# Kernel tuning notes

Measured on AMD Instinct MI355X. Metric: run time of the kernel, lower is better.

Reference implementation:

```python
import jax, jax.numpy as jnp
import numpy as np


def _squash(t, axis):
    # matches torch: t / norm * (norm^2 / (1 + norm^2))
    ns = jnp.sum(t * t, axis=axis, keepdims=True)
    norm = jnp.sqrt(ns)
    return t / norm * (ns / (1.0 + ns))


def setup_inputs() -> dict:
    key = jax.random.key(0)
    k1, k2 = jax.random.split(key)
    B, I, A_IN, O, A_OUT = 16, 2048, 16, 64, 32
    x = jax.random.normal(k1, (B, I, A_IN, 1), dtype=jnp.float32)
    # nn.init.normal(std=0.1)
    weights = jax.random.normal(k2, (I, A_IN, O * A_OUT), dtype=jnp.float32) * 0.1
    # nn.init.constant(val=0.1)
    bias = jnp.full((O, A_OUT), 0.1, dtype=jnp.float32)
    return {"x": x, "weights": weights, "bias": bias}


def reference(x, weights, bias):
    B = x.shape[0]
    I, A_IN, OA = weights.shape
    O, A = bias.shape
    NUM_ROUTING = 3  # hardcoded in the torch forward

    # votes = sum over input_atoms of broadcast(x) * weights  -> [B, I, O, A]
    votes = jnp.einsum('bia,iaj->bij', x[..., 0], weights).reshape(B, I, O, A)
    votes_sg = jax.lax.stop_gradient(votes)

    logits = jnp.zeros((B, I, O), dtype=votes.dtype)
    activation = None
    for i in range(NUM_ROUTING):
        route = jax.nn.softmax(logits, axis=2)  # over output_dim
        v = votes if i == NUM_ROUTING - 1 else votes_sg
        # weighted sum over input capsules: [B, O, A]
        preactivate = jnp.einsum('bio,bioa->boa', route, v) + bias
        activation = _squash(preactivate, axis=2)
        if i < NUM_ROUTING - 1:
            # agreement between votes and current output capsules
            distances = jnp.einsum('bioa,boa->bio', votes, activation)
            logits = logits + distances
    return activation
```

## Files before the change

### kernel.cpp

```cpp
#include <hip/hip_runtime.h>
#include <math.h>

#define B_   16
#define I_   2048
#define AIN_ 16
#define O_   64
#define J_   2048
#define JP_  1024

__device__ __forceinline__ unsigned bf16rne(float f) {
  unsigned u = __float_as_uint(f);
  return (u + 0x7FFFu + ((u >> 16) & 1u)) >> 16;
}
__device__ __forceinline__ float bf16lo(unsigned p) { return __uint_as_float(p << 16); }
__device__ __forceinline__ float bf16hi(unsigned p) { return __uint_as_float(p & 0xFFFF0000u); }

__device__ __forceinline__ float2 ntload2(const float2* p) {
  union { double d; float2 f; } u;
  u.d = __builtin_nontemporal_load((const double*)p);
  return u.f;
}

__global__ __launch_bounds__(512) void votes_kernel(
    const float* __restrict__ x, const float* __restrict__ W,
    unsigned* __restrict__ votes)
{
  __shared__ float x_lds[8 * B_ * AIN_];
  const int tid = threadIdx.x;
  const int islab = blockIdx.x >> 1, jt = blockIdx.x & 1;
  const int i0 = islab * 8;

  for (int e = tid; e < 8 * B_ * AIN_; e += 512) {
    int b = e >> 7, il = (e >> 4) & 7, a = e & 15;
    x_lds[il * 256 + b * 16 + a] =
        x[(size_t)b * (I_ * AIN_) + (size_t)(i0 + il) * AIN_ + a];
  }
  __syncthreads();

  const float2* __restrict__ Wq = (const float2*)W;
  const int jp = jt * 512 + tid;

  for (int il = 0; il < 8; ++il) {
    const int i = i0 + il;
    const float2* __restrict__ Wi = Wq + (size_t)i * (AIN_ * JP_) + jp;
    const float2* __restrict__ xq = (const float2*)x_lds + il * 128;

    float2 v[16];
    #pragma unroll
    for (int b = 0; b < 16; ++b) v[b] = make_float2(0.f, 0.f);

    #pragma unroll
    for (int a2 = 0; a2 < 8; ++a2) {
      float2 w0 = ntload2(Wi + (size_t)(2 * a2 + 0) * JP_);
      float2 w1 = ntload2(Wi + (size_t)(2 * a2 + 1) * JP_);
      #pragma unroll
      for (int b = 0; b < 16; ++b) {
        float2 xv = xq[b * 8 + a2];
        v[b].x = fmaf(xv.x, w0.x, v[b].x);
        v[b].y = fmaf(xv.x, w0.y, v[b].y);
        v[b].x = fmaf(xv.y, w1.x, v[b].x);
        v[b].y = fmaf(xv.y, w1.y, v[b].y);
      }
    }

    unsigned* __restrict__ vo = votes + (size_t)i * (B_ * JP_) + jp;
    #pragma unroll
    for (int b = 0; b < 16; ++b)
      vo[(size_t)b * JP_] = bf16rne(v[b].x) | (bf16rne(v[b].y) << 16);
  }
}

__global__ __launch_bounds__(256) void reduce0_kernel(
    const unsigned* __restrict__ votes, const float* __restrict__ bias,
    float* __restrict__ act)
{
  __shared__ float2 red[4][64];
  const int b = blockIdx.x >> 4, jt = blockIdx.x & 15;
  const int jl = threadIdx.x & 63, is = threadIdx.x >> 6;
  const int jp = jt * 64 + jl;
  const unsigned* __restrict__ vp = votes + (size_t)b * JP_ + jp;

  float2 s0 = make_float2(0.f, 0.f), s1 = make_float2(0.f, 0.f);
  #pragma unroll 4
  for (int k = 0; k < 512; k += 2) {
    unsigned u0 = vp[(size_t)(is + 4 * k)     * (B_ * JP_)];
    unsigned u1 = vp[(size_t)(is + 4 * k + 4) * (B_ * JP_)];
    s0.x += bf16lo(u0); s0.y += bf16hi(u0);
    s1.x += bf16lo(u1); s1.y += bf16hi(u1);
  }
  red[is][jl] = make_float2(s0.x + s1.x, s0.y + s1.y);
  __syncthreads();

  if (threadIdx.x < 64) {
    float2 r0 = red[0][jl], r1 = red[1][jl], r2 = red[2][jl], r3 = red[3][jl];
    const float2 bq = ((const float2*)bias)[jp];
    float px = (r0.x + r1.x + r2.x + r3.x) * (1.0f / 64.0f) + bq.x;
    float py = (r0.y + r1.y + r2.y + r3.y) * (1.0f / 64.0f) + bq.y;
    float ns = px * px + py * py;
    ns += __shfl_xor(ns, 1);  ns += __shfl_xor(ns, 2);
    ns += __shfl_xor(ns, 4);  ns += __shfl_xor(ns, 8);
    float sc = sqrtf(ns) / (1.0f + ns);
    ((float2*)act)[(size_t)b * JP_ + jp] = make_float2(px * sc, py * sc);
  }
}

template<int PASS>
__global__ __launch_bounds__(512) void route_kernel(
    const uint2* __restrict__ votes2, const float* __restrict__ act_in,
    float* __restrict__ part, float* __restrict__ logits)
{
  __shared__ float d_lds[4 * O_];
  __shared__ float r_lds[4 * O_];

  const int jq = threadIdx.x;
  const int islab = blockIdx.x >> 2, bq = blockIdx.x & 3;
  const int i0 = islab * 8;
  const int o = jq >> 3;
  const int l8 = jq & 7;
  const float4* __restrict__ actq = (const float4*)act_in;

  float4 av[4];
  #pragma unroll
  for (int bb = 0; bb < 4; ++bb)
    av[bb] = actq[(size_t)(bq * 4 + bb) * 512 + jq];

  float4 acc[4];
  #pragma unroll
  for (int bb = 0; bb < 4; ++bb) acc[bb] = make_float4(0.f, 0.f, 0.f, 0.f);

  for (int il = 0; il < 8; ++il) {
    const int i = i0 + il;
    const uint2* __restrict__ vo =
        votes2 + (size_t)i * (B_ * 512) + (size_t)(bq * 4) * 512 + jq;
    uint2 vp[4];
    #pragma unroll
    for (int bb = 0; bb < 4; ++bb) vp[bb] = vo[(size_t)bb * 512];

    #pragma unroll
    for (int bb = 0; bb < 4; ++bb) {
      float c = bf16lo(vp[bb].x) * av[bb].x + bf16hi(vp[bb].x) * av[bb].y
              + bf16lo(vp[bb].y) * av[bb].z + bf16hi(vp[bb].y) * av[bb].w;
      c += __shfl_xor(c, 1);  c += __shfl_xor(c, 2);  c += __shfl_xor(c, 4);
      if (l8 == bb) d_lds[bb * 64 + o] = c;
    }
    __syncthreads();

    if (threadIdx.x < 256) {
      const int bb2 = threadIdx.x >> 6, o2 = threadIdx.x & 63;
      const int b2  = bq * 4 + bb2;
      float ell = d_lds[threadIdx.x];
      if (PASS == 2) ell += logits[((size_t)b2 * I_ + i) * O_ + o2];
      if (PASS == 1) logits[((size_t)b2 * I_ + i) * O_ + o2] = ell;
      float m = ell;
      m = fmaxf(m, __shfl_xor(m, 32)); m = fmaxf(m, __shfl_xor(m, 16));
      m = fmaxf(m, __shfl_xor(m, 8));  m = fmaxf(m, __shfl_xor(m, 4));
      m = fmaxf(m, __shfl_xor(m, 2));  m = fmaxf(m, __shfl_xor(m, 1));
      float e = __expf(ell - m);
      float s = e;
      s += __shfl_xor(s, 32); s += __shfl_xor(s, 16); s += __shfl_xor(s, 8);
      s += __shfl_xor(s, 4);  s += __shfl_xor(s, 2);  s += __shfl_xor(s, 1);
      r_lds[threadIdx.x] = e / s;
    }
    __syncthreads();

    #pragma unroll
    for (int bb = 0; bb < 4; ++bb) {
      float r = r_lds[bb * 64 + o];
      acc[bb].x = fmaf(r, bf16lo(vp[bb].x), acc[bb].x);
      acc[bb].y = fmaf(r, bf16hi(vp[bb].x), acc[bb].y);
      acc[bb].z = fmaf(r, bf16lo(vp[bb].y), acc[bb].z);
      acc[bb].w = fmaf(r, bf16hi(vp[bb].y), acc[bb].w);
    }
  }

  float4* __restrict__ po =
      (float4*)part + (size_t)blockIdx.x * (4 * 512) + jq;
  #pragma unroll
  for (int bb = 0; bb < 4; ++bb)
    po[(size_t)bb * 512] = acc[bb];
}

__global__ __launch_bounds__(256) void reduce_squash(
    const float* __restrict__ part, const float* __restrict__ bias,
    float* __restrict__ out)
{
  const int wave = (blockIdx.x * 256 + threadIdx.x) >> 6;
  const int L = threadIdx.x & 63;
  const int a = L & 31, q = L >> 5;
  const int b = wave >> 6, o = wave & 63;
  const int j = o * 32 + a;
  const float* __restrict__ base = part + (size_t)b * J_ + j;

  float s0 = 0.f, s1 = 0.f;
  #pragma unroll 4
  for (int k = 0; k < 128; k += 2) {
    s0 += base[(size_t)(q * 128 + k)     * (B_ * J_)];
    s1 += base[(size_t)(q * 128 + k + 1) * (B_ * J_)];
  }
  float s = s0 + s1;
  s += __shfl_xor(s, 32);

  float p = s + bias[j];
  float ns = p * p;
  ns += __shfl_xor(ns, 1);  ns += __shfl_xor(ns, 2);
  ns += __shfl_xor(ns, 4);  ns += __shfl_xor(ns, 8);
  ns += __shfl_xor(ns, 16);
  if (L < 32) out[(size_t)b * J_ + j] = p * sqrtf(ns) / (1.0f + ns);
}

template<int PASS>
__global__ __launch_bounds__(1024) void fb_pass_kernel(
    const float* __restrict__ x, const float* __restrict__ W,
    const float* __restrict__ act_in, float* __restrict__ part,
    float* __restrict__ logits)
{
  __shared__ float x_lds[8 * B_ * AIN_];
  __shared__ float d_lds[8 * O_];
  __shared__ float r_lds[8 * O_];
  const int tid = threadIdx.x, blk = blockIdx.x, i0 = blk * 8;
  for (int e = tid; e < 8 * B_ * AIN_; e += 1024) {
    int b = e >> 7, il = (e >> 4) & 7, a = e & 15;
    x_lds[il * 256 + b * 16 + a] =
        x[(size_t)b * (I_ * AIN_) + (size_t)(i0 + il) * AIN_ + a];
  }
  __syncthreads();
  const int og = tid >> 4, lg = tid & 15;
  float2 acc[16];
  #pragma unroll
  for (int b = 0; b < 16; ++b) acc[b] = make_float2(0.f, 0.f);
  const float2* __restrict__ Wq   = (const float2*)W;
  const float2* __restrict__ actq = (const float2*)act_in;
  for (int il = 0; il < 8; ++il) {
    const int i = i0 + il;
    const float2* __restrict__ Wi = Wq + (size_t)i * (AIN_ * JP_);
    const float4* __restrict__ xq = (const float4*)x_lds + il * 64;
    for (int h = 0; h < 2; ++h) {
      float2 v[8];
      #pragma unroll
      for (int bb = 0; bb < 8; ++bb) v[bb] = make_float2(0.f, 0.f);
      #pragma unroll
      for (int a4 = 0; a4 < 4; ++a4) {
        float2 w0 = Wi[(size_t)(a4 * 4 + 0) * JP_ + tid];
        float2 w1 = Wi[(size_t)(a4 * 4 + 1) * JP_ + tid];
        float2 w2 = Wi[(size_t)(a4 * 4 + 2) * JP_ + tid];
        float2 w3 = Wi[(size_t)(a4 * 4 + 3) * JP_ + tid];
        #pragma unroll
        for (int bb = 0; bb < 8; ++bb) {
          float4 xv = xq[(h * 8 + bb) * 4 + a4];
          v[bb].x = fmaf(xv.x, w0.x, v[bb].x); v[bb].y = fmaf(xv.x, w0.y, v[bb].y);
          v[bb].x = fmaf(xv.y, w1.x, v[bb].x); v[bb].y = fmaf(xv.y, w1.y, v[bb].y);
          v[bb].x = fmaf(xv.z, w2.x, v[bb].x); v[bb].y = fmaf(xv.z, w2.y, v[bb].y);
          v[bb].x = fmaf(xv.w, w3.x, v[bb].x); v[bb].y = fmaf(xv.w, w3.y, v[bb].y);
        }
      }
      if (PASS == 0) {
        #pragma unroll
        for (int bb = 0; bb < 8; ++bb) {
          acc[h * 8 + bb].x += v[bb].x; acc[h * 8 + bb].y += v[bb].y;
        }
      } else {
        #pragma unroll
        for (int bb = 0; bb < 8; ++bb) {
          const int b = h * 8 + bb;
          float2 avv = actq[(size_t)b * JP_ + tid];
          float c = v[bb].x * avv.x + v[bb].y * avv.y;
          c += __shfl_xor(c, 1); c += __shfl_xor(c, 2);
          c += __shfl_xor(c, 4); c += __shfl_xor(c, 8);
          if (lg == bb) d_lds[bb * 64 + og] = c;
        }
        __syncthreads();
        if (tid < 512) {
          const int bb2 = tid >> 6, o2 = tid & 63;
          const int b2  = h * 8 + bb2;
          float ell = d_lds[tid];
          if (PASS == 2) ell += logits[((size_t)b2 * I_ + i) * O_ + o2];
          if (PASS == 1) logits[((size_t)b2 * I_ + i) * O_ + o2] = ell;
          float m = ell;
          m = fmaxf(m, __shfl_xor(m, 32)); m = fmaxf(m, __shfl_xor(m, 16));
          m = fmaxf(m, __shfl_xor(m, 8));  m = fmaxf(m, __shfl_xor(m, 4));
          m = fmaxf(m, __shfl_xor(m, 2));  m = fmaxf(m, __shfl_xor(m, 1));
          float e = __expf(ell - m);
          float s = e;
          s += __shfl_xor(s, 32); s += __shfl_xor(s, 16); s += __shfl_xor(s, 8);
          s += __shfl_xor(s, 4);  s += __shfl_xor(s, 2);  s += __shfl_xor(s, 1);
          r_lds[tid] = e / s;
        }
        __syncthreads();
        #pragma unroll
        for (int bb = 0; bb < 8; ++bb) {
          float r = r_lds[bb * 64 + og];
          acc[h * 8 + bb].x = fmaf(r, v[bb].x, acc[h * 8 + bb].x);
          acc[h * 8 + bb].y = fmaf(r, v[bb].y, acc[h * 8 + bb].y);
        }
      }
    }
  }
  const float sc = (PASS == 0) ? (1.0f / 64.0f) : 1.0f;
  #pragma unroll
  for (int b = 0; b < 16; ++b) {
    float2* __restrict__ po = (float2*)part +
        (size_t)blk * (B_ * JP_) + (size_t)b * JP_ + tid;
    *po = make_float2(acc[b].x * sc, acc[b].y * sc);
  }
}

extern "C" void kernel_launch(void* const* d_in, const int* in_sizes, int n_in,
                              void* d_out, int out_size, void* d_ws, size_t ws_size,
                              hipStream_t stream) {
  const float* x    = (const float*)d_in[0];
  const float* W    = (const float*)d_in[1];
  const float* bias = (const float*)d_in[2];
  float* out = (float*)d_out;

  float*    part   = (float*)d_ws;
  float*    act    = part + (size_t)256 * (B_ * J_);
  float*    logits = act + (B_ * J_);
  unsigned* votes  = (unsigned*)(logits + (size_t)B_ * I_ * O_);
  const size_t need = ((size_t)256 * B_ * J_ + B_ * J_ + (size_t)B_ * I_ * O_) * 4
                    + (size_t)I_ * B_ * JP_ * 4;

  if (ws_size >= need) {
    votes_kernel<<<512, 512, 0, stream>>>(x, W, votes);
    reduce0_kernel<<<256, 256, 0, stream>>>(votes, bias, act);
    route_kernel<1><<<1024, 512, 0, stream>>>((const uint2*)votes, act, part, logits);
    reduce_squash<<<256, 256, 0, stream>>>(part, bias, act);
    route_kernel<2><<<1024, 512, 0, stream>>>((const uint2*)votes, act, part, logits);
    reduce_squash<<<256, 256, 0, stream>>>(part, bias, out);
  } else {
    fb_pass_kernel<0><<<256, 1024, 0, stream>>>(x, W, act, part, logits);
    reduce_squash<<<256, 256, 0, stream>>>(part, bias, act);
    fb_pass_kernel<1><<<256, 1024, 0, stream>>>(x, W, act, part, logits);
    reduce_squash<<<256, 256, 0, stream>>>(part, bias, act);
    fb_pass_kernel<2><<<256, 1024, 0, stream>>>(x, W, act, part, logits);
    reduce_squash<<<256, 256, 0, stream>>>(part, bias, out);
  }
}
```

Baseline: 199.0 us.

## Widen grids and vectorize vote loads across votes, route and reduce kernels

The votes kernel now handles 4 input capsules per block instead of 8, so it launches twice as many blocks. The reduce0, route and reduce_squash kernels are reorganised to read votes and partials as 16-byte uint4/float4 vectors. Route blocks shrink to 256 threads covering 2 batches each, and the reductions split work over more blocks with an LDS tree at the end. The aim is more parallelism and wider memory transactions on the bandwidth-bound passes. The cost is more partial-sum blocks and different LDS reduction patterns.

```diff
diff --git a/kernel.cpp b/kernel.cpp
--- a/kernel.cpp
+++ b/kernel.cpp
@@ -25,13 +25,14 @@
     const float* __restrict__ x, const float* __restrict__ W,
     unsigned* __restrict__ votes)
 {
-  __shared__ float x_lds[8 * B_ * AIN_];
+  __shared__ float x_lds[4 * B_ * AIN_];
   const int tid = threadIdx.x;
   const int islab = blockIdx.x >> 1, jt = blockIdx.x & 1;
-  const int i0 = islab * 8;
-
-  for (int e = tid; e < 8 * B_ * AIN_; e += 512) {
-    int b = e >> 7, il = (e >> 4) & 7, a = e & 15;
+  const int i0 = islab * 4;
+
+  for (int e = tid; e < 4 * B_ * AIN_; e += 512) {
+    int b = e >> 5 & 15, il = e >> 9, a = e & 15;
+    il = e >> 8; b = (e >> 4) & 15; a = e & 15;
     x_lds[il * 256 + b * 16 + a] =
         x[(size_t)b * (I_ * AIN_) + (size_t)(i0 + il) * AIN_ + a];
   }
@@ -40,7 +41,7 @@
   const float2* __restrict__ Wq = (const float2*)W;
   const int jp = jt * 512 + tid;
 
-  for (int il = 0; il < 8; ++il) {
+  for (int il = 0; il < 4; ++il) {
     const int i = i0 + il;
     const float2* __restrict__ Wi = Wq + (size_t)i * (AIN_ * JP_) + jp;
     const float2* __restrict__ xq = (const float2*)x_lds + il * 128;
@@ -71,141 +72,157 @@
 }
 
 __global__ __launch_bounds__(256) void reduce0_kernel(
-    const unsigned* __restrict__ votes, const float* __restrict__ bias,
+    const uint4* __restrict__ votes4, const float* __restrict__ bias,
     float* __restrict__ act)
 {
-  __shared__ float2 red[4][64];
-  const int b = blockIdx.x >> 4, jt = blockIdx.x & 15;
-  const int jl = threadIdx.x & 63, is = threadIdx.x >> 6;
-  const int jp = jt * 64 + jl;
-  const unsigned* __restrict__ vp = votes + (size_t)b * JP_ + jp;
-
-  float2 s0 = make_float2(0.f, 0.f), s1 = make_float2(0.f, 0.f);
-  #pragma unroll 4
-  for (int k = 0; k < 512; k += 2) {
-    unsigned u0 = vp[(size_t)(is + 4 * k)     * (B_ * JP_)];
-    unsigned u1 = vp[(size_t)(is + 4 * k + 4) * (B_ * JP_)];
-    s0.x += bf16lo(u0); s0.y += bf16hi(u0);
-    s1.x += bf16lo(u1); s1.y += bf16hi(u1);
-  }
-  red[is][jl] = make_float2(s0.x + s1.x, s0.y + s1.y);
+  __shared__ float red[64][4][8];
+  const int b = blockIdx.x >> 6, o = blockIdx.x & 63;
+  const int t = threadIdx.x, s = t >> 2, q = t & 3;
+  const uint4* __restrict__ vp = votes4 + (size_t)b * 256 + (size_t)(o * 4 + q);
+
+  float a0=0.f,a1=0.f,a2=0.f,a3=0.f,a4=0.f,a5=0.f,a6=0.f,a7=0.f;
+  #pragma unroll 8
+  for (int k = 0; k < 32; ++k) {
+    uint4 u = vp[(size_t)(s + 64 * k) * 4096];
+    a0 += bf16lo(u.x); a1 += bf16hi(u.x);
+    a2 += bf16lo(u.y); a3 += bf16hi(u.y);
+    a4 += bf16lo(u.z); a5 += bf16hi(u.z);
+    a6 += bf16lo(u.w); a7 += bf16hi(u.w);
+  }
+  red[s][q][0]=a0; red[s][q][1]=a1; red[s][q][2]=a2; red[s][q][3]=a3;
+  red[s][q][4]=a4; red[s][q][5]=a5; red[s][q][6]=a6; red[s][q][7]=a7;
   __syncthreads();
 
-  if (threadIdx.x < 64) {
-    float2 r0 = red[0][jl], r1 = red[1][jl], r2 = red[2][jl], r3 = red[3][jl];
-    const float2 bq = ((const float2*)bias)[jp];
-    float px = (r0.x + r1.x + r2.x + r3.x) * (1.0f / 64.0f) + bq.x;
-    float py = (r0.y + r1.y + r2.y + r3.y) * (1.0f / 64.0f) + bq.y;
-    float ns = px * px + py * py;
+  if (t < 32) {
+    const int q2 = t >> 3, e = t & 7;
+    float p = 0.f;
+    for (int s2 = 0; s2 < 64; ++s2) p += red[s2][q2][e];
+    p = p * (1.0f / 64.0f) + bias[o * 32 + q2 * 8 + e];
+    float ns = p * p;
     ns += __shfl_xor(ns, 1);  ns += __shfl_xor(ns, 2);
     ns += __shfl_xor(ns, 4);  ns += __shfl_xor(ns, 8);
-    float sc = sqrtf(ns) / (1.0f + ns);
-    ((float2*)act)[(size_t)b * JP_ + jp] = make_float2(px * sc, py * sc);
+    ns += __shfl_xor(ns, 16);
+    act[(size_t)b * J_ + o * 32 + q2 * 8 + e] = p * sqrtf(ns) / (1.0f + ns);
   }
 }
 
 template<int PASS>
-__global__ __launch_bounds__(512) void route_kernel(
-    const uint2* __restrict__ votes2, const float* __restrict__ act_in,
+__global__ __launch_bounds__(256) void route_kernel(
+    const uint4* __restrict__ votes4, const float* __restrict__ act_in,
     float* __restrict__ part, float* __restrict__ logits)
 {
-  __shared__ float d_lds[4 * O_];
-  __shared__ float r_lds[4 * O_];
-
-  const int jq = threadIdx.x;
-  const int islab = blockIdx.x >> 2, bq = blockIdx.x & 3;
+  __shared__ float d_lds[128];
+  __shared__ float r_lds[128];
+
+  const int t = threadIdx.x;
+  const int islab = blockIdx.x >> 3, bq = blockIdx.x & 7;
   const int i0 = islab * 8;
-  const int o = jq >> 3;
-  const int l8 = jq & 7;
+  const int o = t >> 2, l4 = t & 3;
   const float4* __restrict__ actq = (const float4*)act_in;
 
-  float4 av[4];
-  #pragma unroll
-  for (int bb = 0; bb < 4; ++bb)
-    av[bb] = actq[(size_t)(bq * 4 + bb) * 512 + jq];
-
-  float4 acc[4];
-  #pragma unroll
-  for (int bb = 0; bb < 4; ++bb) acc[bb] = make_float4(0.f, 0.f, 0.f, 0.f);
+  float4 av00 = actq[(size_t)(bq * 2 + 0) * 512 + 2 * t];
+  float4 av01 = actq[(size_t)(bq * 2 + 0) * 512 + 2 * t + 1];
+  float4 av10 = actq[(size_t)(bq * 2 + 1) * 512 + 2 * t];
+  float4 av11 = actq[(size_t)(bq * 2 + 1) * 512 + 2 * t + 1];
+
+  float4 ac00 = make_float4(0,0,0,0), ac01 = make_float4(0,0,0,0);
+  float4 ac10 = make_float4(0,0,0,0), ac11 = make_float4(0,0,0,0);
 
   for (int il = 0; il < 8; ++il) {
     const int i = i0 + il;
-    const uint2* __restrict__ vo =
-        votes2 + (size_t)i * (B_ * 512) + (size_t)(bq * 4) * 512 + jq;
-    uint2 vp[4];
-    #pragma unroll
-    for (int bb = 0; bb < 4; ++bb) vp[bb] = vo[(size_t)bb * 512];
-
-    #pragma unroll
-    for (int bb = 0; bb < 4; ++bb) {
-      float c = bf16lo(vp[bb].x) * av[bb].x + bf16hi(vp[bb].x) * av[bb].y
-              + bf16lo(vp[bb].y) * av[bb].z + bf16hi(vp[bb].y) * av[bb].w;
-      c += __shfl_xor(c, 1);  c += __shfl_xor(c, 2);  c += __shfl_xor(c, 4);
-      if (l8 == bb) d_lds[bb * 64 + o] = c;
-    }
+    float lgv = 0.f;
+    if (PASS == 2 && t < 128)
+      lgv = logits[((size_t)(bq * 2 + (t >> 6)) * I_ + i) * O_ + (t & 63)];
+
+    const uint4* __restrict__ vo =
+        votes4 + (size_t)i * 4096 + (size_t)(bq * 2) * 256 + t;
+    uint4 v0 = vo[0];
+    uint4 v1 = vo[256];
+
+    float c0 = bf16lo(v0.x)*av00.x + bf16hi(v0.x)*av00.y
+             + bf16lo(v0.y)*av00.z + bf16hi(v0.y)*av00.w
+             + bf16lo(v0.z)*av01.x + bf16hi(v0.z)*av01.y
+             + bf16lo(v0.w)*av01.z + bf16hi(v0.w)*av01.w;
+    c0 += __shfl_xor(c0, 1);  c0 += __shfl_xor(c0, 2);
+    float c1 = bf16lo(v1.x)*av10.x + bf16hi(v1.x)*av10.y
+             + bf16lo(v1.y)*av10.z + bf16hi(v1.y)*av10.w
+             + bf16lo(v1.z)*av11.x + bf16hi(v1.z)*av11.y
+             + bf16lo(v1.w)*av11.z + bf16hi(v1.w)*av11.w;
+    c1 += __shfl_xor(c1, 1);  c1 += __shfl_xor(c1, 2);
+    if (l4 == 0) d_lds[o]      = c0;
+    if (l4 == 1) d_lds[64 + o] = c1;
     __syncthreads();
 
-    if (threadIdx.x < 256) {
-      const int bb2 = threadIdx.x >> 6, o2 = threadIdx.x & 63;
-      const int b2  = bq * 4 + bb2;
-      float ell = d_lds[threadIdx.x];
-      if (PASS == 2) ell += logits[((size_t)b2 * I_ + i) * O_ + o2];
-      if (PASS == 1) logits[((size_t)b2 * I_ + i) * O_ + o2] = ell;
+    float ellsave = 0.f;
+    if (t < 128) {
+      float ell = d_lds[t];
+      if (PASS == 2) ell += lgv;
+      ellsave = ell;
       float m = ell;
       m = fmaxf(m, __shfl_xor(m, 32)); m = fmaxf(m, __shfl_xor(m, 16));
       m = fmaxf(m, __shfl_xor(m, 8));  m = fmaxf(m, __shfl_xor(m, 4));
       m = fmaxf(m, __shfl_xor(m, 2));  m = fmaxf(m, __shfl_xor(m, 1));
       float e = __expf(ell - m);
-      float s = e;
-      s += __shfl_xor(s, 32); s += __shfl_xor(s, 16); s += __shfl_xor(s, 8);
-      s += __shfl_xor(s, 4);  s += __shfl_xor(s, 2);  s += __shfl_xor(s, 1);
-      r_lds[threadIdx.x] = e / s;
+      float sd = e;
+      sd += __shfl_xor(sd, 32); sd += __shfl_xor(sd, 16); sd += __shfl_xor(sd, 8);
+      sd += __shfl_xor(sd, 4);  sd += __shfl_xor(sd, 2);  sd += __shfl_xor(sd, 1);
+      r_lds[t] = e / sd;
     }
     __syncthreads();
 
-    #pragma unroll
-    for (int bb = 0; bb < 4; ++bb) {
-      float r = r_lds[bb * 64 + o];
-      acc[bb].x = fmaf(r, bf16lo(vp[bb].x), acc[bb].x);
-      acc[bb].y = fmaf(r, bf16hi(vp[bb].x), acc[bb].y);
-      acc[bb].z = fmaf(r, bf16lo(vp[bb].y), acc[bb].z);
-      acc[bb].w = fmaf(r, bf16hi(vp[bb].y), acc[bb].w);
-    }
+    if (PASS == 1 && t < 128)
+      logits[((size_t)(bq * 2 + (t >> 6)) * I_ + i) * O_ + (t & 63)] = ellsave;
+
+    float r0 = r_lds[o], r1 = r_lds[64 + o];
+    ac00.x = fmaf(r0, bf16lo(v0.x), ac00.x); ac00.y = fmaf(r0, bf16hi(v0.x), ac00.y);
+    ac00.z = fmaf(r0, bf16lo(v0.y), ac00.z); ac00.w = fmaf(r0, bf16hi(v0.y), ac00.w);
+    ac01.x = fmaf(r0, bf16lo(v0.z), ac01.x); ac01.y = fmaf(r0, bf16hi(v0.z), ac01.y);
+    ac01.z = fmaf(r0, bf16lo(v0.w), ac01.z); ac01.w = fmaf(r0, bf16hi(v0.w), ac01.w);
+    ac10.x = fmaf(r1, bf16lo(v1.x), ac10.x); ac10.y = fmaf(r1, bf16hi(v1.x), ac10.y);
+    ac10.z = fmaf(r1, bf16lo(v1.y), ac10.z); ac10.w = fmaf(r1, bf16hi(v1.y), ac10.w);
+    ac11.x = fmaf(r1, bf16lo(v1.z), ac11.x); ac11.y = fmaf(r1, bf16hi(v1.z), ac11.y);
+    ac11.z = fmaf(r1, bf16lo(v1.w), ac11.z); ac11.w = fmaf(r1, bf16hi(v1.w), ac11.w);
   }
 
   float4* __restrict__ po =
-      (float4*)part + (size_t)blockIdx.x * (4 * 512) + jq;
-  #pragma unroll
-  for (int bb = 0; bb < 4; ++bb)
-    po[(size_t)bb * 512] = acc[bb];
+      (float4*)part + (size_t)islab * 8192 + (size_t)(bq * 2) * 512 + 2 * t;
+  po[0]   = ac00;  po[1]   = ac01;
+  po[512] = ac10;  po[513] = ac11;
 }
 
 __global__ __launch_bounds__(256) void reduce_squash(
     const float* __restrict__ part, const float* __restrict__ bias,
     float* __restrict__ out)
 {
-  const int wave = (blockIdx.x * 256 + threadIdx.x) >> 6;
-  const int L = threadIdx.x & 63;
-  const int a = L & 31, q = L >> 5;
-  const int b = wave >> 6, o = wave & 63;
-  const int j = o * 32 + a;
-  const float* __restrict__ base = part + (size_t)b * J_ + j;
-
-  float s0 = 0.f, s1 = 0.f;
-  #pragma unroll 4
-  for (int k = 0; k < 128; k += 2) {
-    s0 += base[(size_t)(q * 128 + k)     * (B_ * J_)];
-    s1 += base[(size_t)(q * 128 + k + 1) * (B_ * J_)];
-  }
-  float s = s0 + s1;
-  s += __shfl_xor(s, 32);
-
-  float p = s + bias[j];
-  float ns = p * p;
-  ns += __shfl_xor(ns, 1);  ns += __shfl_xor(ns, 2);
-  ns += __shfl_xor(ns, 4);  ns += __shfl_xor(ns, 8);
-  ns += __shfl_xor(ns, 16);
-  if (L < 32) out[(size_t)b * J_ + j] = p * sqrtf(ns) / (1.0f + ns);
+  __shared__ float4 red[32][8];
+  const int b = blockIdx.x >> 6, o = blockIdx.x & 63;
+  const int t = threadIdx.x, s = t >> 3, q = t & 7;
+  const float4* __restrict__ base =
+      (const float4*)part + (size_t)b * 512 + o * 8 + q;
+
+  float4 acc = make_float4(0.f, 0.f, 0.f, 0.f);
+  #pragma unroll
+  for (int k = 0; k < 8; ++k) {
+    float4 v = base[(size_t)(s + 32 * k) * 8192];
+    acc.x += v.x; acc.y += v.y; acc.z += v.z; acc.w += v.w;
+  }
+  red[s][q] = acc;
+  __syncthreads();
+
+  if (t < 8) {
+    float4 p = make_float4(0.f, 0.f, 0.f, 0.f);
+    for (int s2 = 0; s2 < 32; ++s2) {
+      float4 v = red[s2][t];
+      p.x += v.x; p.y += v.y; p.z += v.z; p.w += v.w;
+    }
+    float4 bq4 = ((const float4*)bias)[o * 8 + t];
+    p.x += bq4.x; p.y += bq4.y; p.z += bq4.z; p.w += bq4.w;
+    float ns = p.x*p.x + p.y*p.y + p.z*p.z + p.w*p.w;
+    ns += __shfl_xor(ns, 1);  ns += __shfl_xor(ns, 2);  ns += __shfl_xor(ns, 4);
+    float sc = sqrtf(ns) / (1.0f + ns);
+    ((float4*)out)[(size_t)b * 512 + o * 8 + t] =
+        make_float4(p.x*sc, p.y*sc, p.z*sc, p.w*sc);
+  }
 }
 
 template<int PASS>
@@ -320,18 +337,18 @@
                     + (size_t)I_ * B_ * JP_ * 4;
 
   if (ws_size >= need) {
-    votes_kernel<<<512, 512, 0, stream>>>(x, W, votes);
-    reduce0_kernel<<<256, 256, 0, stream>>>(votes, bias, act);
-    route_kernel<1><<<1024, 512, 0, stream>>>((const uint2*)votes, act, part, logits);
-    reduce_squash<<<256, 256, 0, stream>>>(part, bias, act);
-    route_kernel<2><<<1024, 512, 0, stream>>>((const uint2*)votes, act, part, logits);
-    reduce_squash<<<256, 256, 0, stream>>>(part, bias, out);
+    votes_kernel<<<1024, 512, 0, stream>>>(x, W, votes);
+    reduce0_kernel<<<1024, 256, 0, stream>>>((const uint4*)votes, bias, act);
+    route_kernel<1><<<2048, 256, 0, stream>>>((const uint4*)votes, act, part, logits);
+    reduce_squash<<<1024, 256, 0, stream>>>(part, bias, act);
+    route_kernel<2><<<2048, 256, 0, stream>>>((const uint4*)votes, act, part, logits);
+    reduce_squash<<<1024, 256, 0, stream>>>(part, bias, out);
   } else {
     fb_pass_kernel<0><<<256, 1024, 0, stream>>>(x, W, act, part, logits);
-    reduce_squash<<<256, 256, 0, stream>>>(part, bias, act);
+    reduce_squash<<<1024, 256, 0, stream>>>(part, bias, act);
     fb_pass_kernel<1><<<256, 1024, 0, stream>>>(x, W, act, part, logits);
-    reduce_squash<<<256, 256, 0, stream>>>(part, bias, act);
+    reduce_squash<<<1024, 256, 0, stream>>>(part, bias, act);
     fb_pass_kernel<2><<<256, 1024, 0, stream>>>(x, W, act, part, logits);
-    reduce_squash<<<256, 256, 0, stream>>>(part, bias, out);
-  }
-}
+    reduce_squash<<<1024, 256, 0, stream>>>(part, bias, out);
+  }
+}
```

Result: faster. 190.5 us (-4.3%).
